# Kernel optimization log

Hardware: AMD Instinct MI355X
Metric: run time of the kernel (lower is better)

## Reference

```python
import jax, jax.numpy as jnp
import numpy as np

N_NODES = 100000
IN_DIM = 500
HID = 64
N_CLASSES = 47
N_EDGES = 1200000
K_LAYERS = 2


def _spmm_rownorm(edge_index, h, n):
    # Row-normalized D^{-1} A @ h via gather + segment_sum over edge list.
    src, dst = edge_index[0], edge_index[1]
    ones = jnp.ones(src.shape[0], dtype=h.dtype)
    deg = jax.ops.segment_sum(ones, src, num_segments=n)
    inv_deg = 1.0 / jnp.maximum(deg, 1.0)
    msg = h[dst] * inv_deg[src][:, None]  # [E, HID]
    return jax.ops.segment_sum(msg, src, num_segments=n)  # [N, HID]


def setup_inputs() -> dict:
    key = jax.random.key(0)
    ks = jax.random.split(key, 12)
    x = jax.random.normal(ks[0], (N_NODES, IN_DIM), dtype=jnp.float32)
    edge_index_1 = jax.random.randint(ks[1], (2, N_EDGES), 0, N_NODES, dtype=jnp.int32)
    edge_index_2 = jax.random.randint(ks[2], (2, N_EDGES), 0, N_NODES, dtype=jnp.int32)
    s = 0.02
    W_embed = jax.random.normal(ks[3], (IN_DIM, HID), dtype=jnp.float32) * s
    b_embed = jnp.zeros((HID,), dtype=jnp.float32)
    W0 = jax.random.normal(ks[4], (4 * HID, HID), dtype=jnp.float32) * s
    b0 = jnp.zeros((HID,), dtype=jnp.float32)
    W1 = jax.random.normal(ks[5], (4 * HID, HID), dtype=jnp.float32) * s
    b1 = jnp.zeros((HID,), dtype=jnp.float32)
    Wc = jax.random.normal(ks[6], (HID * (K_LAYERS + 1), N_CLASSES), dtype=jnp.float32) * s
    bc = jnp.zeros((N_CLASSES,), dtype=jnp.float32)
    return {"x": x, "edge_index_1": edge_index_1, "edge_index_2": edge_index_2,
            "W_embed": W_embed, "b_embed": b_embed, "W0": W0, "b0": b0,
            "W1": W1, "b1": b1, "Wc": Wc, "bc": bc}


def reference(x, edge_index_1, edge_index_2, W_embed, b_embed, W0, b0, W1, b1, Wc, bc):
    n = x.shape[0]
    r0 = jax.nn.relu(x @ W_embed + b_embed)  # dropout = identity in eval
    reps = [r0]
    r_prev = r0
    for (W, b) in ((W0, b0), (W1, b1)):
        n1 = _spmm_rownorm(edge_index_1, r_prev, n)
        n2 = _spmm_rownorm(edge_index_2, r_prev, n)
        concat = jnp.concatenate([r_prev, n1, r_prev, n2], axis=1)  # ego separation
        r_k = jax.nn.relu(concat @ W + b)
        reps.append(r_k)
        r_prev = r_k
    emb = jnp.concatenate(reps, axis=1)  # [N, HID*(K+1)]
    logits = emb @ Wc + bc
    return logits
```

## Files before the change

kernel.cpp:

```cpp
#include <hip/hip_runtime.h>

namespace {

constexpr int N  = 100000;
constexpr int KD = 500;
constexpr int E  = 1200000;
constexpr int NC = 47;

constexpr int M2  = 2 * N;
constexpr int E2  = 2 * E;
constexpr int NB  = 391;
constexpr int AB  = 586;
constexpr int EBMAX = 8192;

typedef __attribute__((ext_vector_type(8))) short short8;
typedef __attribute__((ext_vector_type(4))) float f32x4;

__device__ __forceinline__ ushort f2bf(float f) {
    union { float f; uint u; } c; c.f = f;
    uint u = c.u + 0x7fffu + ((c.u >> 16) & 1);
    return (ushort)(u >> 16);
}
__device__ __forceinline__ float bflo(uint v) { union { uint u; float f; } c; c.u = v << 16;        return c.f; }
__device__ __forceinline__ float bfhi(uint v) { union { uint u; float f; } c; c.u = v & 0xffff0000u; return c.f; }


__global__ __launch_bounds__(256) void prep_all(const float* __restrict__ We, const float* __restrict__ W0,
                                                const float* __restrict__ W1, const float* __restrict__ Wc,
                                                const float* __restrict__ bc,
                                                int* __restrict__ cursor, ushort* __restrict__ wtE,
                                                ushort* __restrict__ wf0, ushort* __restrict__ wf1,
                                                ushort* __restrict__ wct, float* __restrict__ bcp) {
    int i = blockIdx.x * 256 + threadIdx.x;
    if (i < NB) cursor[i] = i * EBMAX;
    if (i < 64 * 512) {
        int c = i >> 9, k = i & 511;
        wtE[i] = f2bf(k < KD ? We[k * 64 + c] : 0.f);
    }
    if (i < 64 * 192) {
        int c = i / 192, k = i % 192;
        float v0, v1;
        if (k < 64)       { v0 = W0[k * 64 + c] + W0[(128 + k) * 64 + c];
                            v1 = W1[k * 64 + c] + W1[(128 + k) * 64 + c]; }
        else if (k < 128) { v0 = W0[k * 64 + c]; v1 = W1[k * 64 + c]; }
        else              { v0 = W0[(k + 64) * 64 + c]; v1 = W1[(k + 64) * 64 + c]; }
        wf0[i] = f2bf(v0);
        wf1[i] = f2bf(v1);
        wct[i] = f2bf(c < NC ? Wc[k * NC + c] : 0.f);
    }
    if (i < 64) bcp[i] = (i < NC) ? bc[i] : 0.f;
}


__global__ __launch_bounds__(256) void bucket_scatter(const int* __restrict__ src1, const int* __restrict__ dst1,
                                                      const int* __restrict__ src2, const int* __restrict__ dst2,
                                                      int* __restrict__ cursor, uint* __restrict__ ebuf) {
    __shared__ int h[NB];
    __shared__ int claim[NB];
    int t = threadIdx.x;
    int mb[16];
    uint mu[16];
    for (int b = t; b < NB; b += 256) h[b] = 0;
    __syncthreads();
    #pragma unroll
    for (int q = 0; q < 16; ++q) {
        int i = blockIdx.x * 4096 + q * 256 + t;
        if (i < E2) {
            int g = i >= E;
            int idx = i - g * E;
            int s = g ? src2[idx] : src1[idx];
            int d = g ? dst2[idx] : dst1[idx];
            int v = g * N + s;
            mb[q] = v >> 9;
            mu[q] = ((uint)(v & 511) << 17) | (uint)d;
            atomicAdd(&h[mb[q]], 1);
        } else {
            mb[q] = -1;
            mu[q] = 0;
        }
    }
    __syncthreads();
    for (int b = t; b < NB; b += 256)
        claim[b] = h[b] ? atomicAdd(&cursor[b], h[b]) : 0;
    __syncthreads();
    for (int b = t; b < NB; b += 256) h[b] = 0;
    __syncthreads();
    #pragma unroll
    for (int q = 0; q < 16; ++q) {
        if (mb[q] >= 0) {
            int r = atomicAdd(&h[mb[q]], 1);
            ebuf[claim[mb[q]] + r] = mu[q];
        }
    }
}

__global__ __launch_bounds__(256) void csr_finalize(const uint* __restrict__ ebuf, const int* __restrict__ cursor,
                                                    int* __restrict__ rp, int* __restrict__ rpe,
                                                    float* __restrict__ invd, int* __restrict__ col) {
    __shared__ uint eb[EBMAX];
    __shared__ int h[512];
    __shared__ int ex[512];
    __shared__ int ps[256];
    int bid = blockIdx.x;
    int t = threadIdx.x;
    int b0 = bid * EBMAX;
    int cnt = cursor[bid] - b0;
    if (cnt > EBMAX) cnt = EBMAX;
    if (cnt < 0) cnt = 0;
    h[t] = 0; h[t + 256] = 0;
    for (int j = t; j < cnt; j += 256) eb[j] = ebuf[b0 + j];
    __syncthreads();
    for (int j = t; j < cnt; j += 256) atomicAdd(&h[eb[j] >> 17], 1);
    __syncthreads();
    int pv = h[2 * t] + h[2 * t + 1];
    ps[t] = pv;
    __syncthreads();
    for (int off = 1; off < 256; off <<= 1) {
        int xv = (t >= off) ? ps[t - off] : 0;
        __syncthreads();
        ps[t] += xv;
        __syncthreads();
    }
    int e2 = ps[t] - pv;
    ex[2 * t] = e2;
    ex[2 * t + 1] = e2 + h[2 * t];
    __syncthreads();
    #pragma unroll
    for (int q = 0; q < 2; ++q) {
        int k = q * 256 + t;
        int n = bid * 512 + k;
        if (n < M2) {
            int st = b0 + ex[k];
            int dv = h[k];
            rp[n]  = st;
            rpe[n] = st + dv;
            invd[n] = 1.0f / (float)(dv > 1 ? dv : 1);
        }
    }
    __syncthreads();
    for (int j = t; j < cnt; j += 256) {
        uint u = eb[j];
        int ls = u >> 17;
        int r = atomicAdd(&ex[ls], 1);
        col[b0 + r] = (int)(u & 0x1FFFFu) * 384;
    }
}


__device__ __forceinline__ void stageB(const ushort* __restrict__ Wt, int ldw, int k0, short* Bs) {
    const int tid = threadIdx.x;
    #pragma unroll
    for (int i = 0; i < 2; ++i) {
        int idx = tid + i * 256;
        int c = idx >> 3, qc = (idx & 7) * 8;
        uint4 v = *reinterpret_cast<const uint4*>(Wt + (size_t)c * ldw + k0 + qc);
        *reinterpret_cast<uint4*>(Bs + (((c << 6) + qc) ^ ((c & 7) << 3))) = v;
    }
}

__device__ __forceinline__ void mma64(const short* As, const short* Bs, f32x4 acc[2][4]) {
    const int lane = threadIdx.x & 63;
    const int wrow = (threadIdx.x >> 6) * 32;
    const int llo = lane & 15, lhi = lane >> 4;
    #pragma unroll
    for (int kf = 0; kf < 2; ++kf) {
        const int kb = kf * 32 + lhi * 8;
        short8 a[2], b[4];
        #pragma unroll
        for (int m = 0; m < 2; ++m) {
            int r = wrow + m * 16 + llo;
            a[m] = *reinterpret_cast<const short8*>(As + (((r << 6) + kb) ^ ((r & 7) << 3)));
        }
        #pragma unroll
        for (int n = 0; n < 4; ++n) {
            int c = n * 16 + llo;
            b[n] = *reinterpret_cast<const short8*>(Bs + (((c << 6) + kb) ^ ((c & 7) << 3)));
        }
        #pragma unroll
        for (int m = 0; m < 2; ++m)
            #pragma unroll
            for (int n = 0; n < 4; ++n)
                acc[m][n] = __builtin_amdgcn_mfma_f32_16x16x32_bf16(a[m], b[n], acc[m][n], 0, 0, 0);
    }
}

template<bool OUTF32>
__device__ __forceinline__ void epilogue(f32x4 acc[2][4], const float* __restrict__ bias,
                                         void* out, int ldo, int ocols, int relu, int rbase) {
    const int lane = threadIdx.x & 63;
    const int wrow = (threadIdx.x >> 6) * 32;
    #pragma unroll
    for (int m = 0; m < 2; ++m) {
        #pragma unroll
        for (int r = 0; r < 4; ++r) {
            int orow = rbase + wrow + m * 16 + (lane >> 4) * 4 + r;
            if (orow >= N) continue;
            #pragma unroll
            for (int n = 0; n < 4; ++n) {
                int c = n * 16 + (lane & 15);
                float v = acc[m][n][r] + bias[c];
                if (relu) v = fmaxf(v, 0.f);
                if (OUTF32) {
                    if (c < ocols) ((float*)out)[(size_t)orow * ldo + c] = v;
                } else {
                    ((ushort*)out)[(size_t)orow * ldo + c] = f2bf(v);
                }
            }
        }
    }
}


__global__ __launch_bounds__(256) void gemm_embed(const float* __restrict__ x,
                                                  const ushort* __restrict__ WtE,
                                                  const float* __restrict__ bias,
                                                  ushort* __restrict__ out) {
    __shared__ short As[32 * 512];
    __shared__ short Bs[64 * 64];
    const int tid = threadIdx.x;
    const int rbase = blockIdx.x * 32;
    const int r = tid >> 3;
    const int j = tid & 7;
    const int swz = (r & 7) << 3;

    const float* xrow = x + (size_t)(rbase + r) * KD;
    float4 pv[16];
    #pragma unroll
    for (int i = 0; i < 16; ++i) {
        int qc = i * 32 + j * 4;
        float4 v = {0.f, 0.f, 0.f, 0.f};
        if (qc < KD) v = *reinterpret_cast<const float4*>(xrow + qc);
        pv[i] = v;
    }
    #pragma unroll
    for (int i = 0; i < 16; ++i) {
        int qc = i * 32 + j * 4;
        uint2 p;
        p.x = (uint)f2bf(pv[i].x) | ((uint)f2bf(pv[i].y) << 16);
        p.y = (uint)f2bf(pv[i].z) | ((uint)f2bf(pv[i].w) << 16);
        *reinterpret_cast<uint2*>(As + ((r << 9) + (qc ^ swz))) = p;
    }

    const int lane = tid & 63;
    const int w = tid >> 6;
    const int llo = lane & 15, lhi = lane >> 4;
    f32x4 acc[2] = {};
    for (int k0 = 0; k0 < 512; k0 += 64) {
        __syncthreads();
        stageB(WtE, 512, k0, Bs);
        __syncthreads();
        #pragma unroll
        for (int kf = 0; kf < 2; ++kf) {
            const int kbl = kf * 32 + lhi * 8;
            const int kab = k0 + kbl;
            short8 a[2], b;
            #pragma unroll
            for (int m = 0; m < 2; ++m) {
                int ar = m * 16 + llo;
                a[m] = *reinterpret_cast<const short8*>(As + ((ar << 9) + (kab ^ ((ar & 7) << 3))));
            }
            {
                int c = w * 16 + llo;
                b = *reinterpret_cast<const short8*>(Bs + (((c << 6) + kbl) ^ ((c & 7) << 3)));
            }
            #pragma unroll
            for (int m = 0; m < 2; ++m)
                acc[m] = __builtin_amdgcn_mfma_f32_16x16x32_bf16(a[m], b, acc[m], 0, 0, 0);
        }
    }

    #pragma unroll
    for (int m = 0; m < 2; ++m) {
        #pragma unroll
        for (int rr = 0; rr < 4; ++rr) {
            int orow = rbase + m * 16 + lhi * 4 + rr;
            int c = w * 16 + llo;
            float v = acc[m][rr] + bias[c];
            v = fmaxf(v, 0.f);
            out[(size_t)orow * 192 + c] = f2bf(v);
        }
    }
}

template<bool OUTF32>
__global__ __launch_bounds__(256) void gemm3(const ushort* __restrict__ a0, int lda0,
                                             const ushort* __restrict__ a1, int lda1,
                                             const ushort* __restrict__ a2, int lda2,
                                             const ushort* __restrict__ Wt,
                                             const float* __restrict__ bias,
                                             void* out, int ldo, int ocols, int relu) {
    __shared__ short As[128 * 64];
    __shared__ short Bs[64 * 64];
    const int tid = threadIdx.x;
    const int rbase = blockIdx.x * 128;
    f32x4 acc[2][4] = {};
    const ushort* aseg[3] = {a0, a1, a2};
    const int ldas[3] = {lda0, lda1, lda2};
    #pragma unroll
    for (int seg = 0; seg < 3; ++seg) {
        const ushort* A = aseg[seg];
        const int lda = ldas[seg];
        __syncthreads();
        #pragma unroll
        for (int i = 0; i < 4; ++i) {
            int idx = tid + i * 256;
            int r = idx >> 3, qc = (idx & 7) * 8;
            int grow = rbase + r;
            uint4 v = {0u, 0u, 0u, 0u};
            if (grow < N) v = *reinterpret_cast<const uint4*>(A + (size_t)grow * lda + qc);
            *reinterpret_cast<uint4*>(As + (((r << 6) + qc) ^ ((r & 7) << 3))) = v;
        }
        stageB(Wt, 192, seg * 64, Bs);
        __syncthreads();
        mma64(As, Bs, acc);
    }
    epilogue<OUTF32>(acc, bias, out, ldo, ocols, relu, rbase);
}


__global__ __launch_bounds__(256) void spmm7(const int* __restrict__ rp, const int* __restrict__ rpe,
                                             const int* __restrict__ col,
                                             const float* __restrict__ invd,
                                             const ushort* __restrict__ table, int colOff,
                                             ushort* __restrict__ n1b, ushort* __restrict__ n2b) {
    int gid = (blockIdx.x * 256 + threadIdx.x) >> 3;
    int ls = threadIdx.x & 7;
    if (gid >= M2) return;
    const char* hb = (const char*)(table + colOff) + ls * 16;
    float w = invd[gid];
    int s = rp[gid], e = rpe[gid];
    int e1 = e - 1;
    float a0=0.f,a1=0.f,a2=0.f,a3=0.f,a4=0.f,a5=0.f,a6=0.f,a7=0.f;
    for (int j = s; j < e; j += 8) {
        int off[8];
        float wv[8];
        #pragma unroll
        for (int u = 0; u < 8; ++u) {
            int jj = j + u;
            int cidx = jj < e ? jj : e1;
            off[u] = col[cidx];
            wv[u] = jj < e ? 1.f : 0.f;
        }
        uint4 v[8];
        #pragma unroll
        for (int u = 0; u < 8; ++u) v[u] = *reinterpret_cast<const uint4*>(hb + off[u]);
        #pragma unroll
        for (int u = 0; u < 8; ++u) {
            a0 = fmaf(wv[u], bflo(v[u].x), a0); a1 = fmaf(wv[u], bfhi(v[u].x), a1);
            a2 = fmaf(wv[u], bflo(v[u].y), a2); a3 = fmaf(wv[u], bfhi(v[u].y), a3);
            a4 = fmaf(wv[u], bflo(v[u].z), a4); a5 = fmaf(wv[u], bfhi(v[u].z), a5);
            a6 = fmaf(wv[u], bflo(v[u].w), a6); a7 = fmaf(wv[u], bfhi(v[u].w), a7);
        }
    }
    int g = gid >= N;
    int node = gid - g * N;
    ushort* op = g ? n2b : n1b;
    uint4 o;
    o.x = (uint)f2bf(a0 * w) | ((uint)f2bf(a1 * w) << 16);
    o.y = (uint)f2bf(a2 * w) | ((uint)f2bf(a3 * w) << 16);
    o.z = (uint)f2bf(a4 * w) | ((uint)f2bf(a5 * w) << 16);
    o.w = (uint)f2bf(a6 * w) | ((uint)f2bf(a7 * w) << 16);
    *reinterpret_cast<uint4*>(op + (size_t)node * 64 + ls * 8) = o;
}

}

extern "C" void kernel_launch(void* const* d_in, const int* in_sizes, int n_in,
                              void* d_out, int out_size, void* d_ws, size_t ws_size,
                              hipStream_t stream) {
    const float* x       = (const float*)d_in[0];
    const int*   ei1     = (const int*)d_in[1];
    const int*   ei2     = (const int*)d_in[2];
    const float* W_embed = (const float*)d_in[3];
    const float* b_embed = (const float*)d_in[4];
    const float* W0      = (const float*)d_in[5];
    const float* b0      = (const float*)d_in[6];
    const float* W1      = (const float*)d_in[7];
    const float* b1      = (const float*)d_in[8];
    const float* Wc      = (const float*)d_in[9];
    const float* bc      = (const float*)d_in[10];
    float* out = (float*)d_out;

    char* ws = (char*)d_ws;
    size_t off = 0;
    auto alloc = [&](size_t bytes) -> void* {
        void* p = ws + off;
        off += (bytes + 255) & ~(size_t)255;
        return p;
    };

    ushort* embB  = (ushort*)alloc((size_t)N * 192 * 2);
    ushort* n1b   = (ushort*)alloc((size_t)N * 64 * 2);
    ushort* n2b   = (ushort*)alloc((size_t)N * 64 * 2);
    int*    col   = (int*)alloc((size_t)NB * EBMAX * 4);
    uint*   ebuf  = (uint*)alloc((size_t)NB * EBMAX * 4);
    int*    rp    = (int*)alloc((size_t)M2 * 4);
    int*    rpe   = (int*)alloc((size_t)M2 * 4);
    float*  invd  = (float*)alloc((size_t)M2 * 4);
    int*    bcur  = (int*)alloc((NB + 1) * 4);
    ushort* wtE   = (ushort*)alloc(64 * 512 * 2);
    ushort* weff0 = (ushort*)alloc(64 * 192 * 2);
    ushort* weff1 = (ushort*)alloc(64 * 192 * 2);
    ushort* wct   = (ushort*)alloc(64 * 192 * 2);
    float*  bcp   = (float*)alloc(64 * 4);
    if (off > ws_size) return;

    const int* src1 = ei1, *dst1 = ei1 + E;
    const int* src2 = ei2, *dst2 = ei2 + E;

    const int GB  = (N + 127) / 128;
    const int GBE = N / 32;
    const int PB  = (M2 * 8 + 255) / 256;

    prep_all<<<128, 256, 0, stream>>>(W_embed, W0, W1, Wc, bc, bcur, wtE, weff0, weff1, wct, bcp);

    bucket_scatter<<<AB, 256, 0, stream>>>(src1, dst1, src2, dst2, bcur, ebuf);
    csr_finalize<<<NB, 256, 0, stream>>>(ebuf, bcur, rp, rpe, invd, col);

    gemm_embed<<<GBE, 256, 0, stream>>>(x, wtE, b_embed, embB);

    for (int layer = 0; layer < 2; ++layer) {
        const ushort* rprev = embB + 64 * layer;
        spmm7<<<PB, 256, 0, stream>>>(rp, rpe, col, invd, embB, 64 * layer, n1b, n2b);
        const ushort* Wl = (layer == 0) ? weff0 : weff1;
        const float*  bl = (layer == 0) ? b0 : b1;
        gemm3<false><<<GB, 256, 0, stream>>>(rprev, 192, n1b, 64, n2b, 64, Wl, bl,
                                             embB + 64 * (layer + 1), 192, 64, 1);
    }

    gemm3<true><<<GB, 256, 0, stream>>>(embB, 192, embB + 64, 192, embB + 128, 192, wct, bcp,
                                        out, NC, NC, 0);
}
```

Measured before the change: 223.6 us.

## Fuse layer-1 GEMM with classifier, merge prep into scatter, shrink embedding stride

```diff
diff --git a/kernel.cpp b/kernel.cpp
--- a/kernel.cpp
+++ b/kernel.cpp
@@ -11,7 +11,9 @@
 constexpr int E2  = 2 * E;
 constexpr int NB  = 391;
 constexpr int AB  = 586;
+constexpr int PREPB = 128;
 constexpr int EBMAX = 8192;
+constexpr int LDE = 128;
 
 typedef __attribute__((ext_vector_type(8))) short short8;
 typedef __attribute__((ext_vector_type(4))) float f32x4;
@@ -25,71 +27,71 @@
 __device__ __forceinline__ float bfhi(uint v) { union { uint u; float f; } c; c.u = v & 0xffff0000u; return c.f; }
 
 
-__global__ __launch_bounds__(256) void prep_all(const float* __restrict__ We, const float* __restrict__ W0,
-                                                const float* __restrict__ W1, const float* __restrict__ Wc,
-                                                const float* __restrict__ bc,
-                                                int* __restrict__ cursor, ushort* __restrict__ wtE,
-                                                ushort* __restrict__ wf0, ushort* __restrict__ wf1,
-                                                ushort* __restrict__ wct, float* __restrict__ bcp) {
-    int i = blockIdx.x * 256 + threadIdx.x;
-    if (i < NB) cursor[i] = i * EBMAX;
-    if (i < 64 * 512) {
-        int c = i >> 9, k = i & 511;
-        wtE[i] = f2bf(k < KD ? We[k * 64 + c] : 0.f);
-    }
-    if (i < 64 * 192) {
-        int c = i / 192, k = i % 192;
-        float v0, v1;
-        if (k < 64)       { v0 = W0[k * 64 + c] + W0[(128 + k) * 64 + c];
-                            v1 = W1[k * 64 + c] + W1[(128 + k) * 64 + c]; }
-        else if (k < 128) { v0 = W0[k * 64 + c]; v1 = W1[k * 64 + c]; }
-        else              { v0 = W0[(k + 64) * 64 + c]; v1 = W1[(k + 64) * 64 + c]; }
-        wf0[i] = f2bf(v0);
-        wf1[i] = f2bf(v1);
-        wct[i] = f2bf(c < NC ? Wc[k * NC + c] : 0.f);
-    }
-    if (i < 64) bcp[i] = (i < NC) ? bc[i] : 0.f;
-}
-
-
-__global__ __launch_bounds__(256) void bucket_scatter(const int* __restrict__ src1, const int* __restrict__ dst1,
-                                                      const int* __restrict__ src2, const int* __restrict__ dst2,
-                                                      int* __restrict__ cursor, uint* __restrict__ ebuf) {
+__global__ __launch_bounds__(256) void prep_scatter(
+        const float* __restrict__ We, const float* __restrict__ W0,
+        const float* __restrict__ W1, const float* __restrict__ Wc,
+        const float* __restrict__ bc,
+        const int* __restrict__ src1, const int* __restrict__ dst1,
+        const int* __restrict__ src2, const int* __restrict__ dst2,
+        int* __restrict__ cursor, uint* __restrict__ ebuf,
+        ushort* __restrict__ wtE, ushort* __restrict__ wf0, ushort* __restrict__ wf1,
+        ushort* __restrict__ wct, float* __restrict__ bcp) {
     __shared__ int h[NB];
     __shared__ int claim[NB];
-    int t = threadIdx.x;
-    int mb[16];
-    uint mu[16];
-    for (int b = t; b < NB; b += 256) h[b] = 0;
-    __syncthreads();
-    #pragma unroll
-    for (int q = 0; q < 16; ++q) {
-        int i = blockIdx.x * 4096 + q * 256 + t;
-        if (i < E2) {
-            int g = i >= E;
-            int idx = i - g * E;
-            int s = g ? src2[idx] : src1[idx];
-            int d = g ? dst2[idx] : dst1[idx];
-            int v = g * N + s;
-            mb[q] = v >> 9;
-            mu[q] = ((uint)(v & 511) << 17) | (uint)d;
-            atomicAdd(&h[mb[q]], 1);
-        } else {
-            mb[q] = -1;
-            mu[q] = 0;
-        }
-    }
-    __syncthreads();
-    for (int b = t; b < NB; b += 256)
-        claim[b] = h[b] ? atomicAdd(&cursor[b], h[b]) : 0;
-    __syncthreads();
-    for (int b = t; b < NB; b += 256) h[b] = 0;
-    __syncthreads();
-    #pragma unroll
-    for (int q = 0; q < 16; ++q) {
-        if (mb[q] >= 0) {
-            int r = atomicAdd(&h[mb[q]], 1);
-            ebuf[claim[mb[q]] + r] = mu[q];
+    const int t = threadIdx.x;
+    if (blockIdx.x < PREPB) {
+        int i = blockIdx.x * 256 + t;
+        if (i < 64 * 512) {
+            int c = i >> 9, k = i & 511;
+            wtE[i] = f2bf(k < KD ? We[k * 64 + c] : 0.f);
+        }
+        if (i < 64 * 192) {
+            int c = i / 192, k = i % 192;
+            float v0, v1;
+            if (k < 64)       { v0 = W0[k * 64 + c] + W0[(128 + k) * 64 + c];
+                                v1 = W1[k * 64 + c] + W1[(128 + k) * 64 + c]; }
+            else if (k < 128) { v0 = W0[k * 64 + c]; v1 = W1[k * 64 + c]; }
+            else              { v0 = W0[(k + 64) * 64 + c]; v1 = W1[(k + 64) * 64 + c]; }
+            wf0[i] = f2bf(v0);
+            wf1[i] = f2bf(v1);
+            wct[i] = f2bf(c < NC ? Wc[k * NC + c] : 0.f);
+        }
+        if (i < 64) bcp[i] = (i < NC) ? bc[i] : 0.f;
+    } else {
+        const int blk = blockIdx.x - PREPB;
+        int mb[16];
+        uint mu[16];
+        for (int b = t; b < NB; b += 256) h[b] = 0;
+        __syncthreads();
+        #pragma unroll
+        for (int q = 0; q < 16; ++q) {
+            int i = blk * 4096 + q * 256 + t;
+            if (i < E2) {
+                int g = i >= E;
+                int idx = i - g * E;
+                int s = g ? src2[idx] : src1[idx];
+                int d = g ? dst2[idx] : dst1[idx];
+                int v = g * N + s;
+                mb[q] = v >> 9;
+                mu[q] = ((uint)(v & 511) << 17) | (uint)d;
+                atomicAdd(&h[mb[q]], 1);
+            } else {
+                mb[q] = -1;
+                mu[q] = 0;
+            }
+        }
+        __syncthreads();
+        for (int b = t; b < NB; b += 256)
+            claim[b] = h[b] ? atomicAdd(&cursor[b], h[b]) : 0;
+        __syncthreads();
+        for (int b = t; b < NB; b += 256) h[b] = 0;
+        __syncthreads();
+        #pragma unroll
+        for (int q = 0; q < 16; ++q) {
+            if (mb[q] >= 0) {
+                int r = atomicAdd(&h[mb[q]], 1);
+                ebuf[(size_t)mb[q] * EBMAX + claim[mb[q]] + r] = mu[q];
+            }
         }
     }
 }
@@ -104,7 +106,7 @@
     int bid = blockIdx.x;
     int t = threadIdx.x;
     int b0 = bid * EBMAX;
-    int cnt = cursor[bid] - b0;
+    int cnt = cursor[bid];
     if (cnt > EBMAX) cnt = EBMAX;
     if (cnt < 0) cnt = 0;
     h[t] = 0; h[t + 256] = 0;
@@ -142,7 +144,7 @@
         uint u = eb[j];
         int ls = u >> 17;
         int r = atomicAdd(&ex[ls], 1);
-        col[b0 + r] = (int)(u & 0x1FFFFu) * 384;
+        col[b0 + r] = (int)(u & 0x1FFFFu) * 256;
     }
 }
 
@@ -277,18 +279,18 @@
             int c = w * 16 + llo;
             float v = acc[m][rr] + bias[c];
             v = fmaxf(v, 0.f);
-            out[(size_t)orow * 192 + c] = f2bf(v);
-        }
-    }
-}
-
-template<bool OUTF32>
+            out[(size_t)orow * LDE + c] = f2bf(v);
+        }
+    }
+}
+
+
 __global__ __launch_bounds__(256) void gemm3(const ushort* __restrict__ a0, int lda0,
                                              const ushort* __restrict__ a1, int lda1,
                                              const ushort* __restrict__ a2, int lda2,
                                              const ushort* __restrict__ Wt,
                                              const float* __restrict__ bias,
-                                             void* out, int ldo, int ocols, int relu) {
+                                             ushort* __restrict__ out, int ldo) {
     __shared__ short As[128 * 64];
     __shared__ short Bs[64 * 64];
     const int tid = threadIdx.x;
@@ -314,7 +316,86 @@
         __syncthreads();
         mma64(As, Bs, acc);
     }
-    epilogue<OUTF32>(acc, bias, out, ldo, ocols, relu, rbase);
+    epilogue<false>(acc, bias, out, ldo, 64, 1, rbase);
+}
+
+
+__global__ __launch_bounds__(256) void gemm_l1cls(const ushort* __restrict__ embB,
+                                                  const ushort* __restrict__ n1b,
+                                                  const ushort* __restrict__ n2b,
+                                                  const ushort* __restrict__ W1t,
+                                                  const float* __restrict__ b1,
+                                                  const ushort* __restrict__ Wct,
+                                                  const float* __restrict__ bcp,
+                                                  float* __restrict__ out) {
+    __shared__ short As[128 * 64];
+    __shared__ short Bs1[64 * 64];
+    __shared__ short Bs2[64 * 64];
+    const int tid = threadIdx.x;
+    const int rbase = blockIdx.x * 128;
+    f32x4 acc1[2][4] = {};
+    f32x4 acc2[2][4] = {};
+
+    auto stageA = [&](const ushort* A, int lda) {
+        #pragma unroll
+        for (int i = 0; i < 4; ++i) {
+            int idx = tid + i * 256;
+            int r = idx >> 3, qc = (idx & 7) * 8;
+            int grow = rbase + r;
+            uint4 v = {0u, 0u, 0u, 0u};
+            if (grow < N) v = *reinterpret_cast<const uint4*>(A + (size_t)grow * lda + qc);
+            *reinterpret_cast<uint4*>(As + (((r << 6) + qc) ^ ((r & 7) << 3))) = v;
+        }
+    };
+
+    stageA(embB + 64, LDE);
+    stageB(W1t, 192, 0, Bs1);
+    stageB(Wct, 192, 64, Bs2);
+    __syncthreads();
+    mma64(As, Bs1, acc1);
+    mma64(As, Bs2, acc2);
+    __syncthreads();
+
+    stageA(n1b, 64);
+    stageB(W1t, 192, 64, Bs1);
+    __syncthreads();
+    mma64(As, Bs1, acc1);
+    __syncthreads();
+
+    stageA(n2b, 64);
+    stageB(W1t, 192, 128, Bs1);
+    __syncthreads();
+    mma64(As, Bs1, acc1);
+    __syncthreads();
+
+    {
+        const int lane = tid & 63;
+        const int wrow = (tid >> 6) * 32;
+        #pragma unroll
+        for (int m = 0; m < 2; ++m) {
+            #pragma unroll
+            for (int r = 0; r < 4; ++r) {
+                int row = wrow + m * 16 + (lane >> 4) * 4 + r;
+                #pragma unroll
+                for (int n = 0; n < 4; ++n) {
+                    int c = n * 16 + (lane & 15);
+                    float v = fmaxf(acc1[m][n][r] + b1[c], 0.f);
+                    As[(((row << 6) + c) ^ ((row & 7) << 3))] = (short)f2bf(v);
+                }
+            }
+        }
+    }
+    stageB(Wct, 192, 128, Bs1);
+    __syncthreads();
+    mma64(As, Bs1, acc2);
+    __syncthreads();
+
+    stageA(embB, LDE);
+    stageB(Wct, 192, 0, Bs1);
+    __syncthreads();
+    mma64(As, Bs1, acc2);
+
+    epilogue<true>(acc2, bcp, out, NC, NC, 0, rbase);
 }
 
 
@@ -389,7 +470,7 @@
         return p;
     };
 
-    ushort* embB  = (ushort*)alloc((size_t)N * 192 * 2);
+    ushort* embB  = (ushort*)alloc((size_t)N * LDE * 2);
     ushort* n1b   = (ushort*)alloc((size_t)N * 64 * 2);
     ushort* n2b   = (ushort*)alloc((size_t)N * 64 * 2);
     int*    col   = (int*)alloc((size_t)NB * EBMAX * 4);
@@ -412,22 +493,19 @@
     const int GBE = N / 32;
     const int PB  = (M2 * 8 + 255) / 256;
 
-    prep_all<<<128, 256, 0, stream>>>(W_embed, W0, W1, Wc, bc, bcur, wtE, weff0, weff1, wct, bcp);
-
-    bucket_scatter<<<AB, 256, 0, stream>>>(src1, dst1, src2, dst2, bcur, ebuf);
+    hipMemsetAsync(bcur, 0, NB * sizeof(int), stream);
+
+    prep_scatter<<<PREPB + AB, 256, 0, stream>>>(W_embed, W0, W1, Wc, bc,
+                                                 src1, dst1, src2, dst2, bcur, ebuf,
+                                                 wtE, weff0, weff1, wct, bcp);
+
     csr_finalize<<<NB, 256, 0, stream>>>(ebuf, bcur, rp, rpe, invd, col);
 
     gemm_embed<<<GBE, 256, 0, stream>>>(x, wtE, b_embed, embB);
 
-    for (int layer = 0; layer < 2; ++layer) {
-        const ushort* rprev = embB + 64 * layer;
-        spmm7<<<PB, 256, 0, stream>>>(rp, rpe, col, invd, embB, 64 * layer, n1b, n2b);
-        const ushort* Wl = (layer == 0) ? weff0 : weff1;
-        const float*  bl = (layer == 0) ? b0 : b1;
-        gemm3<false><<<GB, 256, 0, stream>>>(rprev, 192, n1b, 64, n2b, 64, Wl, bl,
-                                             embB + 64 * (layer + 1), 192, 64, 1);
-    }
-
-    gemm3<true><<<GB, 256, 0, stream>>>(embB, 192, embB + 64, 192, embB + 128, 192, wct, bcp,
-                                        out, NC, NC, 0);
-}
+    spmm7<<<PB, 256, 0, stream>>>(rp, rpe, col, invd, embB, 0, n1b, n2b);
+    gemm3<<<GB, 256, 0, stream>>>(embB, LDE, n1b, 64, n2b, 64, weff0, b0, embB + 64, LDE);
+
+    spmm7<<<PB, 256, 0, stream>>>(rp, rpe, col, invd, embB, 64, n1b, n2b);
+    gemm_l1cls<<<GB, 256, 0, stream>>>(embB, n1b, n2b, weff1, b1, wct, bcp, out);
+}
```

Result: faster. 218.5 us, median of 2 (-2.3%).
